# Optimization experiments

Hardware: AMD Instinct MI355X
Metric: run time of the kernel (lower is better)

## Reference

```python
import jax, jax.numpy as jnp
import numpy as np

N = 41616      # 16 graphs * 51*51 nodes
E = 249696     # 6 * N edges
C = 128        # channel_conv
K = 6          # Chebyshev order
H = 32         # hidden_size
NB = 18        # 6 blocks * 3 ChebConvs


def _prop(x, src, dst, w):
    # one application of scaled Laplacian L_hat: gather -> weight -> scatter-add
    return jax.ops.segment_sum(w[:, None] * x[src], dst, num_segments=N)


def _cheb(x, W, b, src, dst, w):
    # PyG ChebConv: out = sum_k T_k(L_hat) x @ W_k + b, recurrence T_k = 2 L T_{k-1} - T_{k-2}
    Tx0 = x
    out = Tx0 @ W[0]
    Tx1 = _prop(Tx0, src, dst, w)
    out = out + Tx1 @ W[1]
    for k in range(2, W.shape[0]):
        Tx2 = 2.0 * _prop(Tx1, src, dst, w) - Tx0
        out = out + Tx2 @ W[k]
        Tx0, Tx1 = Tx1, Tx2
    return out + b


def setup_inputs() -> dict:
    key = jax.random.key(0)
    ks = jax.random.split(key, 10)
    glorot = lambda k, sh: jax.random.normal(k, sh, jnp.float32) * (2.0 / (sh[-2] + sh[-1])) ** 0.5
    inp = {}
    inp["vector"] = jax.random.normal(ks[0], (16, H), jnp.float32)
    inp["edges"] = jax.random.randint(ks[1], (2, E), 0, N)
    inp["sphere_pos"] = jax.random.normal(ks[2], (N, 3), jnp.float32)
    inp["fc1_w"] = glorot(ks[3], (H, 128)); inp["fc1_b"] = jnp.zeros((128,), jnp.float32)
    inp["fc2_w"] = glorot(ks[4], (128, 51 * 51 * 6)); inp["fc2_b"] = jnp.zeros((51 * 51 * 6,), jnp.float32)
    inp["Wi"] = glorot(ks[5], (K, 9, C)); inp["bi"] = jnp.zeros((C,), jnp.float32)
    inp["Wb"] = glorot(ks[6], (NB, K, C, C)); inp["bb"] = jnp.zeros((NB, C), jnp.float32)
    inp["Wf"] = glorot(ks[7], (K, C, 3)); inp["bf"] = jnp.zeros((3,), jnp.float32)
    return inp


def reference(vector, edges, sphere_pos, fc1_w, fc1_b, fc2_w, fc2_b, Wi, bi, Wb, bb, Wf, bf):
    src, dst = edges[0], edges[1]
    # sym-normalized scaled Laplacian with lambda_max=2: L_hat = -D^{-1/2} A D^{-1/2}
    deg = jax.ops.segment_sum(jnp.ones((E,), jnp.float32), dst, num_segments=N)
    dinv = jnp.where(deg > 0, jax.lax.rsqrt(jnp.maximum(deg, 1.0)), 0.0)
    w = -dinv[src] * dinv[dst]

    v = jax.nn.relu(vector @ fc1_w + fc1_b)
    v = jax.nn.relu(v @ fc2_w + fc2_b)
    v = v.reshape(-1, 6)                              # [N, 6]
    x = jnp.concatenate([sphere_pos, v], axis=1)      # [N, 9]
    x = _cheb(x, Wi, bi, src, dst, w)                 # [N, C]
    for i in range(6):
        res = x
        for j in range(3):
            x = jax.nn.relu(_cheb(x, Wb[3 * i + j], bb[3 * i + j], src, dst, w))
        x = x + res
    x = _cheb(x, Wf, bf, src, dst, w)                 # [N, 3]
    return jnp.tanh(x)
```

## Files before the change

kernel.cpp:

```cpp
#include <hip/hip_runtime.h>
#include <cstdio>

#define N_NODES 41616
#define N_EDGES 249696
#define WLO_OFF ((size_t)108 * 16384)

typedef __attribute__((ext_vector_type(8))) short short8v;
typedef __attribute__((ext_vector_type(4))) float f32x4;

__device__ inline unsigned short f2bf_rne(float f) {
  unsigned int u = __builtin_bit_cast(unsigned int, f);
  u += 0x7fffu + ((u >> 16) & 1u);
  return (unsigned short)(u >> 16);
}


__global__ void k_deg(const int* __restrict__ dst, int* __restrict__ deg) {
  int e = blockIdx.x * 256 + threadIdx.x;
  if (e < N_EDGES) atomicAdd(&deg[dst[e]], 1);
}

__global__ void k_dinv(const int* __restrict__ deg, float* __restrict__ dinv) {
  int n = blockIdx.x * 256 + threadIdx.x;
  if (n < N_NODES) {
    int d = deg[n];
    dinv[n] = d > 0 ? rsqrtf((float)d) : 0.f;
  }
}

__global__ void k_blocksum(const int* __restrict__ deg, int* __restrict__ bsum) {
  __shared__ int s[256];
  int b = blockIdx.x, tid = threadIdx.x;
  int base = b * 1024;
  int acc = 0;
  for (int j = 0; j < 4; ++j) {
    int i = base + j * 256 + tid;
    if (i < N_NODES) acc += deg[i];
  }
  s[tid] = acc;
  __syncthreads();
  for (int off = 128; off > 0; off >>= 1) {
    if (tid < off) s[tid] += s[tid + off];
    __syncthreads();
  }
  if (tid == 0) bsum[b] = s[0];
}

__global__ void k_scan_bsum(const int* __restrict__ bsum, int* __restrict__ boff,
                            int nb, int* __restrict__ row_off) {
  if (threadIdx.x == 0 && blockIdx.x == 0) {
    int run = 0;
    for (int j = 0; j < nb; ++j) { boff[j] = run; run += bsum[j]; }
    row_off[N_NODES] = run;
  }
}

__global__ void k_scan_chunk(const int* __restrict__ deg, const int* __restrict__ boff,
                             int* __restrict__ row_off) {
  __shared__ int s[1024];
  int b = blockIdx.x, tid = threadIdx.x;
  int i = b * 1024 + tid;
  int v = (i < N_NODES) ? deg[i] : 0;
  s[tid] = v;
  __syncthreads();
  for (int off = 1; off < 1024; off <<= 1) {
    int t = (tid >= off) ? s[tid - off] : 0;
    __syncthreads();
    s[tid] += t;
    __syncthreads();
  }
  if (i < N_NODES) row_off[i] = boff[b] + s[tid] - v;
}

__global__ void k_fill(const int* __restrict__ src, const int* __restrict__ dst,
                       const float* __restrict__ dinv, const int* __restrict__ row_off,
                       int* __restrict__ cursor, int* __restrict__ esrc,
                       float* __restrict__ ew) {
  int e = blockIdx.x * 256 + threadIdx.x;
  if (e >= N_EDGES) return;
  int d = dst[e], sn = src[e];
  int pos = atomicAdd(&cursor[d], 1);
  int o = row_off[d] + pos;
  esrc[o] = sn;
  ew[o] = -dinv[sn] * dinv[d];
}


__global__ void k_wswz(const float* __restrict__ W, unsigned short* __restrict__ Wsw,
                       int total) {
  int idx = blockIdx.x * 256 + threadIdx.x;
  if (idx >= total) return;
  int t = idx >> 14, r = idx & 16383;
  int k = r >> 7, col = r & 127;
  int kstep = k >> 5, kin = k & 31, g = kin >> 3, j = kin & 7;
  int ct = col >> 4, lc = col & 15, lane = g * 16 + lc;
  size_t dst = ((size_t)t << 14) + (size_t)((kstep * 8 + ct) * 64 + lane) * 8 + j;
  float x = W[idx];
  unsigned short h = f2bf_rne(x);
  float hv = __builtin_bit_cast(float, (unsigned int)h << 16);
  Wsw[dst] = h;
  Wsw[WLO_OFF + dst] = f2bf_rne(x - hv);
}


__global__ void k_mlp1(const float* __restrict__ vec, const float* __restrict__ w1,
                       const float* __restrict__ b1, float* __restrict__ v1) {
  int idx = blockIdx.x * 256 + threadIdx.x;
  if (idx >= 16 * 128) return;
  int g = idx >> 7, j = idx & 127;
  float acc = b1[j];
  for (int i = 0; i < 32; ++i) acc += vec[g * 32 + i] * w1[i * 128 + j];
  v1[idx] = fmaxf(acc, 0.f);
}

__global__ void k_mlp2(const float* __restrict__ v1, const float* __restrict__ w2,
                       const float* __restrict__ b2, float* __restrict__ x0) {
  __shared__ float sv[2048];
  int tid = threadIdx.x;
  for (int i = tid; i < 2048; i += 256) sv[i] = v1[i];
  __syncthreads();
  int r = blockIdx.x * 256 + tid;
  if (r >= 15606) return;
  float bb = b2[r];
  float acc[16];
#pragma unroll
  for (int g = 0; g < 16; ++g) acc[g] = bb;
  for (int i = 0; i < 128; ++i) {
    float wv = w2[i * 15606 + r];
#pragma unroll
    for (int g = 0; g < 16; ++g) acc[g] += sv[g * 128 + i] * wv;
  }
  int q = r / 6, cc = r - q * 6;
#pragma unroll
  for (int g = 0; g < 16; ++g) {
    int node = g * 2601 + q;
    x0[node * 9 + 3 + cc] = fmaxf(acc[g], 0.f);
  }
}

__global__ void k_pos(const float* __restrict__ sp, float* __restrict__ x0) {
  int idx = blockIdx.x * 256 + threadIdx.x;
  if (idx >= N_NODES * 3) return;
  int n = idx / 3, c = idx - n * 3;
  x0[n * 9 + c] = sp[idx];
}


template <int CC>
__global__ void k_prop(const float* __restrict__ x, const float* __restrict__ prev,
                       float* __restrict__ out, const int* __restrict__ row_off,
                       const int* __restrict__ esrc, const float* __restrict__ ew,
                       float alpha, float beta) {
  int idx = blockIdx.x * 256 + threadIdx.x;
  if (idx >= N_NODES * CC) return;
  int n = idx / CC, c = idx - n * CC;
  int e0 = row_off[n], e1 = row_off[n + 1];
  float acc = 0.f;
  for (int e = e0; e < e1; ++e) acc += ew[e] * x[esrc[e] * CC + c];
  float o = alpha * acc;
  if (beta != 0.f) o += beta * prev[idx];
  out[idx] = o;
}

__global__ __launch_bounds__(256) void k_prop128v(
    const float* __restrict__ x, const float* __restrict__ prev, float* __restrict__ out,
    const int* __restrict__ row_off, const int* __restrict__ esrc,
    const float* __restrict__ ew, float alpha, float beta) {
  int tid = threadIdx.x;
  int lane = tid & 31;
  int n = blockIdx.x * 8 + (tid >> 5);
  if (n >= N_NODES) return;
  int e0 = row_off[n], e1 = row_off[n + 1];
  const float4* xv = (const float4*)x;
  float4 acc = {0.f, 0.f, 0.f, 0.f};
  int e = e0;
  for (; e + 4 <= e1; e += 4) {
    int s0 = esrc[e], s1 = esrc[e + 1], s2 = esrc[e + 2], s3 = esrc[e + 3];
    float w0 = ew[e], w1 = ew[e + 1], w2 = ew[e + 2], w3 = ew[e + 3];
    float4 v0 = xv[(size_t)s0 * 32 + lane];
    float4 v1 = xv[(size_t)s1 * 32 + lane];
    float4 v2 = xv[(size_t)s2 * 32 + lane];
    float4 v3 = xv[(size_t)s3 * 32 + lane];
    acc.x += w0 * v0.x + w1 * v1.x + w2 * v2.x + w3 * v3.x;
    acc.y += w0 * v0.y + w1 * v1.y + w2 * v2.y + w3 * v3.y;
    acc.z += w0 * v0.z + w1 * v1.z + w2 * v2.z + w3 * v3.z;
    acc.w += w0 * v0.w + w1 * v1.w + w2 * v2.w + w3 * v3.w;
  }
  for (; e < e1; ++e) {
    float w = ew[e];
    float4 v = xv[(size_t)esrc[e] * 32 + lane];
    acc.x += w * v.x; acc.y += w * v.y; acc.z += w * v.z; acc.w += w * v.w;
  }
  size_t oidx = (size_t)n * 32 + lane;
  float4 o = {alpha * acc.x, alpha * acc.y, alpha * acc.z, alpha * acc.w};
  if (beta != 0.f) {
    float4 p = ((const float4*)prev)[oidx];
    o.x += beta * p.x; o.y += beta * p.y; o.z += beta * p.z; o.w += beta * p.w;
  }
  ((float4*)out)[oidx] = o;
}


__global__ __launch_bounds__(256) void k_gemm3m(
    const float* __restrict__ Ta, const float* __restrict__ Tb, const float* __restrict__ Tc,
    const unsigned short* __restrict__ Wsw, float* __restrict__ OUT,
    const float* __restrict__ bias, const float* __restrict__ res, int flags) {
  int tid = threadIdx.x;
  int lane = tid & 63;
  int w = tid >> 6;
  int row0 = blockIdx.x * 64;
  int arow = row0 + w * 16 + (lane & 15);
  int arowc = arow < N_NODES ? arow : N_NODES - 1;
  size_t abase = (size_t)arowc * 128 + (lane >> 4) * 8;

  f32x4 acc[8];
#pragma unroll
  for (int i = 0; i < 8; ++i) acc[i] = (f32x4){0.f, 0.f, 0.f, 0.f};

#pragma unroll
  for (int t = 0; t < 3; ++t) {
    const float* A = (t == 0) ? Ta : (t == 1) ? Tb : Tc;
    const uint4* Whi = (const uint4*)(Wsw + ((size_t)t << 14));
    const uint4* Wlo = (const uint4*)(Wsw + WLO_OFF + ((size_t)t << 14));
    float4 a0[4], a1[4];
#pragma unroll
    for (int s = 0; s < 4; ++s) {
      const float4* ap = (const float4*)(A + abase + s * 32);
      a0[s] = ap[0];
      a1[s] = ap[1];
    }
    short8v ahi[4], alo[4];
#pragma unroll
    for (int s = 0; s < 4; ++s) {
      float av[8] = {a0[s].x, a0[s].y, a0[s].z, a0[s].w,
                     a1[s].x, a1[s].y, a1[s].z, a1[s].w};
#pragma unroll
      for (int j = 0; j < 8; ++j) {
        unsigned short h = f2bf_rne(av[j]);
        ahi[s][j] = (short)h;
        float hv = __builtin_bit_cast(float, (unsigned int)h << 16);
        alo[s][j] = (short)f2bf_rne(av[j] - hv);
      }
    }
#pragma unroll
    for (int s = 0; s < 4; ++s) {
#pragma unroll
      for (int ct = 0; ct < 8; ++ct) {
        int wi = (s * 8 + ct) * 64 + lane;
        short8v bhi = __builtin_bit_cast(short8v, Whi[wi]);
        short8v blo = __builtin_bit_cast(short8v, Wlo[wi]);
        acc[ct] = __builtin_amdgcn_mfma_f32_16x16x32_bf16(ahi[s], bhi, acc[ct], 0, 0, 0);
        acc[ct] = __builtin_amdgcn_mfma_f32_16x16x32_bf16(ahi[s], blo, acc[ct], 0, 0, 0);
        acc[ct] = __builtin_amdgcn_mfma_f32_16x16x32_bf16(alo[s], bhi, acc[ct], 0, 0, 0);
      }
    }
  }

  int rbase = row0 + w * 16 + (lane >> 4) * 4;
  int cbase = lane & 15;
#pragma unroll
  for (int ct = 0; ct < 8; ++ct) {
#pragma unroll
    for (int r = 0; r < 4; ++r) {
      int gr = rbase + r;
      if (gr >= N_NODES) continue;
      int col = ct * 16 + cbase;
      float v = acc[ct][r];
      float* dp = OUT + (size_t)gr * 128 + col;
      if (!(flags & 1)) v += *dp;
      if (flags & 2) v += bias[col];
      if (flags & 4) v = fmaxf(v, 0.f);
      if (flags & 8) v += res[(size_t)gr * 128 + col];
      *dp = v;
    }
  }
}

__global__ __launch_bounds__(256) void k_gemm9f(
    const float* __restrict__ T0, const float* __restrict__ T1, const float* __restrict__ T2,
    const float* __restrict__ T3, const float* __restrict__ T4, const float* __restrict__ T5,
    const float* __restrict__ Wi, const float* __restrict__ bi, float* __restrict__ OUT) {
  __shared__ float sA[2][54];
  __shared__ const float* sT[6];
  int tid = threadIdx.x;
  int n0 = blockIdx.x * 2;
  if (tid == 0) { sT[0] = T0; sT[1] = T1; sT[2] = T2; sT[3] = T3; sT[4] = T4; sT[5] = T5; }
  __syncthreads();
  if (tid < 108) {
    int nl = tid / 54, q = tid % 54;
    int n = n0 + nl;
    sA[nl][q] = (n < N_NODES) ? sT[q / 9][(size_t)n * 9 + (q % 9)] : 0.f;
  }
  __syncthreads();
  int nl = tid >> 7, c = tid & 127;
  int n = n0 + nl;
  if (n >= N_NODES) return;
  float acc = bi[c];
#pragma unroll
  for (int q = 0; q < 54; ++q) acc += sA[nl][q] * Wi[q * 128 + c];
  OUT[(size_t)n * 128 + c] = acc;
}

__global__ __launch_bounds__(256) void k_gemv3(
    const float* __restrict__ A, const float* __restrict__ W, float* __restrict__ OUT,
    const float* __restrict__ bias, int flags) {
  __shared__ float As[64][129];
  int node0 = blockIdx.x * 64;
  int tid = threadIdx.x;
#pragma unroll
  for (int i = 0; i < 32; ++i) {
    int idx = tid + i * 256;
    int r = idx >> 7, cc = idx & 127;
    int gn = node0 + r;
    As[r][cc] = (gn < N_NODES) ? A[(size_t)gn * 128 + cc] : 0.f;
  }
  __syncthreads();
  if (tid >= 192) return;
  int ln = tid / 3, c = tid - ln * 3;
  int gn = node0 + ln;
  if (gn >= N_NODES) return;
  float acc = (flags & 1) ? 0.f : OUT[(size_t)gn * 3 + c];
  for (int k = 0; k < 128; ++k) acc += As[ln][k] * W[k * 3 + c];
  if (flags & 2) acc = tanhf(acc + bias[c]);
  OUT[(size_t)gn * 3 + c] = acc;
}


extern "C" void kernel_launch(void* const* d_in, const int* in_sizes, int n_in,
                              void* d_out, int out_size, void* d_ws, size_t ws_size,
                              hipStream_t stream) {
  const float* vec = (const float*)d_in[0];
  const int* edges = (const int*)d_in[1];
  const float* sp  = (const float*)d_in[2];
  const float* w1  = (const float*)d_in[3];
  const float* b1  = (const float*)d_in[4];
  const float* w2  = (const float*)d_in[5];
  const float* b2  = (const float*)d_in[6];
  const float* Wi  = (const float*)d_in[7];
  const float* bi  = (const float*)d_in[8];
  const float* Wb  = (const float*)d_in[9];
  const float* bbp = (const float*)d_in[10];
  const float* Wf  = (const float*)d_in[11];
  const float* bf  = (const float*)d_in[12];
  float* out = (float*)d_out;

  const int* src = edges;
  const int* dst = edges + N_EDGES;

  size_t off = 0;
  auto alloc = [&](size_t bytes) -> void* {
    size_t o = (off + 255) & ~(size_t)255;
    off = o + bytes;
    return (void*)((char*)d_ws + o);
  };
  int* deg      = (int*)alloc((size_t)N_NODES * 4);
  float* dinv   = (float*)alloc((size_t)N_NODES * 4);
  int* row_off  = (int*)alloc((size_t)(N_NODES + 1) * 4);
  int* cursor   = (int*)alloc((size_t)N_NODES * 4);
  int* bsum     = (int*)alloc(64 * 4);
  int* boff     = (int*)alloc(64 * 4);
  int* esrc     = (int*)alloc((size_t)N_EDGES * 4);
  float* ew     = (float*)alloc((size_t)N_EDGES * 4);
  float* v1     = (float*)alloc(2048 * 4);
  unsigned short* wsw = (unsigned short*)alloc((size_t)2 * 108 * 16384 * 2);
  float* B[6];
  for (int i = 0; i < 6; ++i) B[i] = (float*)alloc((size_t)N_NODES * 128 * 4);
  if (off > ws_size) {
    fprintf(stderr, "kernel_launch: ws too small (need %zu, have %zu)\n", off, ws_size);
    return;
  }
  float* PA = B[3];
  float* PB = B[4];
  float* PC = B[5];
  const size_t X9 = (size_t)N_NODES * 9;
  float* x0 = B[1];
  float* t9[5];
  for (int i = 0; i < 5; ++i) t9[i] = B[1] + (size_t)(i + 1) * X9;

  const int NCH = (N_NODES + 1023) / 1024;
  hipMemsetAsync(deg, 0, (size_t)N_NODES * 4, stream);
  hipMemsetAsync(cursor, 0, (size_t)N_NODES * 4, stream);
  k_deg<<<(N_EDGES + 255) / 256, 256, 0, stream>>>(dst, deg);
  k_dinv<<<(N_NODES + 255) / 256, 256, 0, stream>>>(deg, dinv);
  k_blocksum<<<NCH, 256, 0, stream>>>(deg, bsum);
  k_scan_bsum<<<1, 64, 0, stream>>>(bsum, boff, NCH, row_off);
  k_scan_chunk<<<NCH, 1024, 0, stream>>>(deg, boff, row_off);
  k_fill<<<(N_EDGES + 255) / 256, 256, 0, stream>>>(src, dst, dinv, row_off, cursor, esrc, ew);

  const int WTOT = 108 * 16384;
  k_wswz<<<(WTOT + 255) / 256, 256, 0, stream>>>(Wb, wsw, WTOT);

  k_mlp1<<<8, 256, 0, stream>>>(vec, w1, b1, v1);
  k_mlp2<<<(15606 + 255) / 256, 256, 0, stream>>>(v1, w2, b2, x0);
  k_pos<<<(N_NODES * 3 + 255) / 256, 256, 0, stream>>>(sp, x0);

  const int gP9  = (N_NODES * 9 + 255) / 256;
  const int gPn  = (N_NODES + 7) / 8;
  const int gG64 = (N_NODES + 63) / 64;
  const int g2   = (N_NODES + 1) / 2;

  k_prop<9><<<gP9, 256, 0, stream>>>(x0, x0, t9[0], row_off, esrc, ew, 1.f, 0.f);
  k_prop<9><<<gP9, 256, 0, stream>>>(t9[0], x0, t9[1], row_off, esrc, ew, 2.f, -1.f);
  k_prop<9><<<gP9, 256, 0, stream>>>(t9[1], t9[0], t9[2], row_off, esrc, ew, 2.f, -1.f);
  k_prop<9><<<gP9, 256, 0, stream>>>(t9[2], t9[1], t9[3], row_off, esrc, ew, 2.f, -1.f);
  k_prop<9><<<gP9, 256, 0, stream>>>(t9[3], t9[2], t9[4], row_off, esrc, ew, 2.f, -1.f);
  k_gemm9f<<<g2, 256, 0, stream>>>(x0, t9[0], t9[1], t9[2], t9[3], t9[4], Wi, bi, B[0]);

  auto cheb128 = [&](const float* in, const unsigned short* Wk, const float* bk,
                     float* OUTb, const float* resb, int lastflags) {
    k_prop128v<<<gPn, 256, 0, stream>>>(in, in, PA, row_off, esrc, ew, 1.f, 0.f);
    k_prop128v<<<gPn, 256, 0, stream>>>(PA, in, PB, row_off, esrc, ew, 2.f, -1.f);
    k_gemm3m<<<gG64, 256, 0, stream>>>(in, PA, PB, Wk, OUTb, bk, nullptr, 1 | 2);
    k_prop128v<<<gPn, 256, 0, stream>>>(PB, PA, PC, row_off, esrc, ew, 2.f, -1.f);
    k_prop128v<<<gPn, 256, 0, stream>>>(PC, PB, PA, row_off, esrc, ew, 2.f, -1.f);
    k_prop128v<<<gPn, 256, 0, stream>>>(PA, PC, PB, row_off, esrc, ew, 2.f, -1.f);
    k_gemm3m<<<gG64, 256, 0, stream>>>(PC, PA, PB, Wk + 3 * 16384, OUTb, bk, resb, lastflags);
  };

  float* cur = B[0];
  float* s1 = B[1];
  float* s2 = B[2];
  for (int blk = 0; blk < 6; ++blk) {
    const float* resb = cur;
    const unsigned short* W0 = wsw + (size_t)(3 * blk + 0) * 6 * 16384;
    const unsigned short* W1 = wsw + (size_t)(3 * blk + 1) * 6 * 16384;
    const unsigned short* W2 = wsw + (size_t)(3 * blk + 2) * 6 * 16384;
    cheb128(cur, W0, bbp + (3 * blk + 0) * 128, s1, nullptr, 4);
    cheb128(s1, W1, bbp + (3 * blk + 1) * 128, s2, nullptr, 4);
    cheb128(s2, W2, bbp + (3 * blk + 2) * 128, s1, resb, 4 | 8);
    float* tmp = cur; cur = s1; s1 = tmp;
  }

  k_gemv3<<<gG64, 256, 0, stream>>>(cur, Wf + 0 * 384, out, bf, 1);
  k_prop128v<<<gPn, 256, 0, stream>>>(cur, cur, PA, row_off, esrc, ew, 1.f, 0.f);
  k_gemv3<<<gG64, 256, 0, stream>>>(PA, Wf + 1 * 384, out, bf, 0);
  k_prop128v<<<gPn, 256, 0, stream>>>(PA, cur, PB, row_off, esrc, ew, 2.f, -1.f);
  k_gemv3<<<gG64, 256, 0, stream>>>(PB, Wf + 2 * 384, out, bf, 0);
  k_prop128v<<<gPn, 256, 0, stream>>>(PB, PA, PA, row_off, esrc, ew, 2.f, -1.f);
  k_gemv3<<<gG64, 256, 0, stream>>>(PA, Wf + 3 * 384, out, bf, 0);
  k_prop128v<<<gPn, 256, 0, stream>>>(PA, PB, PB, row_off, esrc, ew, 2.f, -1.f);
  k_gemv3<<<gG64, 256, 0, stream>>>(PB, Wf + 4 * 384, out, bf, 0);
  k_prop128v<<<gPn, 256, 0, stream>>>(PB, PA, PA, row_off, esrc, ew, 2.f, -1.f);
  k_gemv3<<<gG64, 256, 0, stream>>>(PA, Wf + 5 * 384, out, bf, 2);
}
```

Measured before the change: 3.881 ms.

## Split GEMM K dimension across wave pairs with LDS reduction

The 3-term Chebyshev GEMM kernel now gives each block 32 rows instead of 64, and splits the 128-wide K dimension between two pairs of waves. The upper-half waves write their partial accumulators to shared memory and exit, and the lower-half waves add them before running the epilogue. This doubles the grid and halves the serial MFMA chain per wave, which should improve latency hiding and occupancy. The cost is an LDS round trip, a block barrier, and half the waves sitting idle during the epilogue.

```diff
diff --git a/kernel.cpp b/kernel.cpp
--- a/kernel.cpp
+++ b/kernel.cpp
@@ -205,13 +205,15 @@
     const float* __restrict__ Ta, const float* __restrict__ Tb, const float* __restrict__ Tc,
     const unsigned short* __restrict__ Wsw, float* __restrict__ OUT,
     const float* __restrict__ bias, const float* __restrict__ res, int flags) {
+  __shared__ uint4 ldsP[1024];
   int tid = threadIdx.x;
   int lane = tid & 63;
   int w = tid >> 6;
-  int row0 = blockIdx.x * 64;
-  int arow = row0 + w * 16 + (lane & 15);
+  int rg = w & 1, kh = w >> 1;
+  int row0 = blockIdx.x * 32 + rg * 16;
+  int arow = row0 + (lane & 15);
   int arowc = arow < N_NODES ? arow : N_NODES - 1;
-  size_t abase = (size_t)arowc * 128 + (lane >> 4) * 8;
+  size_t abase = (size_t)arowc * 128 + kh * 64 + (lane >> 4) * 8;
 
   f32x4 acc[8];
 #pragma unroll
@@ -222,16 +224,16 @@
     const float* A = (t == 0) ? Ta : (t == 1) ? Tb : Tc;
     const uint4* Whi = (const uint4*)(Wsw + ((size_t)t << 14));
     const uint4* Wlo = (const uint4*)(Wsw + WLO_OFF + ((size_t)t << 14));
-    float4 a0[4], a1[4];
-#pragma unroll
-    for (int s = 0; s < 4; ++s) {
+    float4 a0[2], a1[2];
+#pragma unroll
+    for (int s = 0; s < 2; ++s) {
       const float4* ap = (const float4*)(A + abase + s * 32);
       a0[s] = ap[0];
       a1[s] = ap[1];
     }
-    short8v ahi[4], alo[4];
-#pragma unroll
-    for (int s = 0; s < 4; ++s) {
+    short8v ahi[2], alo[2];
+#pragma unroll
+    for (int s = 0; s < 2; ++s) {
       float av[8] = {a0[s].x, a0[s].y, a0[s].z, a0[s].w,
                      a1[s].x, a1[s].y, a1[s].z, a1[s].w};
 #pragma unroll
@@ -243,10 +245,11 @@
       }
     }
 #pragma unroll
-    for (int s = 0; s < 4; ++s) {
+    for (int s = 0; s < 2; ++s) {
+      int S = kh * 2 + s;
 #pragma unroll
       for (int ct = 0; ct < 8; ++ct) {
-        int wi = (s * 8 + ct) * 64 + lane;
+        int wi = (S * 8 + ct) * 64 + lane;
         short8v bhi = __builtin_bit_cast(short8v, Whi[wi]);
         short8v blo = __builtin_bit_cast(short8v, Wlo[wi]);
         acc[ct] = __builtin_amdgcn_mfma_f32_16x16x32_bf16(ahi[s], bhi, acc[ct], 0, 0, 0);
@@ -256,7 +259,21 @@
     }
   }
 
-  int rbase = row0 + w * 16 + (lane >> 4) * 4;
+  if (kh == 1) {
+#pragma unroll
+    for (int ct = 0; ct < 8; ++ct)
+      ldsP[rg * 512 + ct * 64 + lane] = __builtin_bit_cast(uint4, acc[ct]);
+  }
+  __syncthreads();
+  if (kh == 1) return;
+
+#pragma unroll
+  for (int ct = 0; ct < 8; ++ct) {
+    f32x4 p = __builtin_bit_cast(f32x4, ldsP[rg * 512 + ct * 64 + lane]);
+    acc[ct] += p;
+  }
+
+  int rbase = row0 + (lane >> 4) * 4;
   int cbase = lane & 15;
 #pragma unroll
   for (int ct = 0; ct < 8; ++ct) {
@@ -396,6 +413,7 @@
 
   const int gP9  = (N_NODES * 9 + 255) / 256;
   const int gPn  = (N_NODES + 7) / 8;
+  const int gG32 = (N_NODES + 31) / 32;
   const int gG64 = (N_NODES + 63) / 64;
   const int g2   = (N_NODES + 1) / 2;
 
@@ -410,11 +428,11 @@
                      float* OUTb, const float* resb, int lastflags) {
     k_prop128v<<<gPn, 256, 0, stream>>>(in, in, PA, row_off, esrc, ew, 1.f, 0.f);
     k_prop128v<<<gPn, 256, 0, stream>>>(PA, in, PB, row_off, esrc, ew, 2.f, -1.f);
-    k_gemm3m<<<gG64, 256, 0, stream>>>(in, PA, PB, Wk, OUTb, bk, nullptr, 1 | 2);
+    k_gemm3m<<<gG32, 256, 0, stream>>>(in, PA, PB, Wk, OUTb, bk, nullptr, 1 | 2);
     k_prop128v<<<gPn, 256, 0, stream>>>(PB, PA, PC, row_off, esrc, ew, 2.f, -1.f);
     k_prop128v<<<gPn, 256, 0, stream>>>(PC, PB, PA, row_off, esrc, ew, 2.f, -1.f);
     k_prop128v<<<gPn, 256, 0, stream>>>(PA, PC, PB, row_off, esrc, ew, 2.f, -1.f);
-    k_gemm3m<<<gG64, 256, 0, stream>>>(PC, PA, PB, Wk + 3 * 16384, OUTb, bk, resb, lastflags);
+    k_gemm3m<<<gG32, 256, 0, stream>>>(PC, PA, PB, Wk + 3 * 16384, OUTb, bk, resb, lastflags);
   };
 
   float* cur = B[0];
```

After: 4.129 ms. 1.06x slower.
